# Performance work log

Hardware: AMD Instinct MI355X
Metric: run time of the kernel (lower is better)

## Reference

```python
import jax, jax.numpy as jnp
import numpy as np

N, F, K = 2048, 256, 4
E = 65536

def setup_inputs() -> dict:
    key = jax.random.key(0)
    ks = jax.random.split(key, 8)
    batch_x = jax.random.normal(ks[0], (N, F), dtype=jnp.float32)
    # eigen-matrix of a normalized Laplacian is diagonal in practice, but the
    # original code treats it as a dense [N,N] operand; we mimic a diagonal
    # eigenvalue matrix (eigenvalues in [0,2]) -- math is identical either way.
    lam_diag = 2.0 * jax.random.uniform(ks[1], (N,), dtype=jnp.float32)
    batch_lam = jnp.diag(lam_diag)
    batch_U = jax.random.normal(ks[2], (N, N), dtype=jnp.float32) / jnp.sqrt(jnp.float32(N))
    # init.uniform_(a, 0, 2) / (b, 0, 2) / (c, -1, 1); keep a-b bounded away from 0
    a_list = 1.0 + jax.random.uniform(ks[3], (K,), dtype=jnp.float32)        # [1,2)
    b_list = 0.9 * jax.random.uniform(ks[4], (K,), dtype=jnp.float32)       # [0,0.9)
    c_list = 2.0 * jax.random.uniform(ks[5], (K,), dtype=jnp.float32) - 1.0  # [-1,1)
    residual_alpha = jnp.ones((1,), dtype=jnp.float32)
    edge_index = jax.random.randint(ks[6], (2, E), 0, N, dtype=jnp.int64)
    return {"batch_x": batch_x, "batch_lam": batch_lam, "batch_U": batch_U,
            "a_list": a_list, "b_list": b_list, "c_list": c_list,
            "residual_alpha": residual_alpha, "edge_index": edge_index}

def reference(batch_x, batch_lam, batch_U, a_list, b_list, c_list, residual_alpha, edge_index):
    n = batch_lam.shape[0]
    I = jnp.eye(n, dtype=batch_lam.dtype)
    out = residual_alpha * batch_x  # residual added at hop 0 in original
    for i in range(a_list.shape[0]):
        # filter_rep = (a_i*I - Lam) @ (Lam - b_i*I), then relu
        rep = (a_list[i] * I - batch_lam) @ (batch_lam - b_list[i] * I)
        rep = jax.nn.relu(rep)
        scale = c_list[i] / ((a_list[i] - b_list[i]) * (a_list[i] - b_list[i]) / 4.0)
        filt = scale * (batch_U @ (rep @ (batch_U.T @ batch_x)))
        out = out + filt
    return out
```

## Files before the change

kernel.cpp:

```cpp
#include <hip/hip_runtime.h>
#include <type_traits>

typedef unsigned short u16;
typedef __attribute__((ext_vector_type(8))) short short8;
typedef __attribute__((ext_vector_type(4))) float floatx4;

__device__ __forceinline__ u16 f2u(float f) {
  unsigned int x = __float_as_uint(f);
  x += 0x7fff + ((x >> 16) & 1);
  return (u16)(x >> 16);
}

__device__ __forceinline__ void async16(const void* g, void* l) {
  __builtin_amdgcn_global_load_lds(
      (const __attribute__((address_space(1))) unsigned int*)g,
      (__attribute__((address_space(3))) unsigned int*)l, 16, 0, 0);
}

__global__ __launch_bounds__(256) void prep_kernel(
    const float* __restrict__ U, const float* __restrict__ x,
    u16* __restrict__ Ut, u16* __restrict__ Ubf, u16* __restrict__ xT,
    int N, int F) {
  __shared__ __attribute__((aligned(16))) float tile[64][65];
  int bb = blockIdx.x;
  int t = threadIdx.x;

  const float* in;
  u16 *outT, *outC;
  int R, C, c0, r0;
  if (bb < 1024) {
    in = U; outT = Ut; outC = Ubf; R = N; C = N;
    c0 = (bb & 31) * 64; r0 = (bb >> 5) * 64;
  } else {
    int b2 = bb - 1024;
    in = x; outT = xT; outC = nullptr; R = N; C = F;
    c0 = (b2 & 3) * 64; r0 = (b2 >> 2) * 64;
  }

#pragma unroll
  for (int p = 0; p < 4; ++p) {
    int e = p * 256 + t;
    int row = e >> 4, col = (e & 15) * 4;
    float4 v = *(const float4*)(in + (size_t)(r0 + row) * C + c0 + col);
    tile[row][col] = v.x;
    tile[row][col + 1] = v.y;
    tile[row][col + 2] = v.z;
    tile[row][col + 3] = v.w;
    if (outC) {
      union { uint2 u; u16 s[4]; } pk;
      pk.s[0] = f2u(v.x); pk.s[1] = f2u(v.y);
      pk.s[2] = f2u(v.z); pk.s[3] = f2u(v.w);
      *(uint2*)(outC + (size_t)(r0 + row) * C + c0 + col) = pk.u;
    }
  }
  __syncthreads();
#pragma unroll
  for (int p = 0; p < 2; ++p) {
    int e = p * 256 + t;
    int orow = e >> 3, oc = (e & 7) * 8;
    union { uint4 v; u16 s[8]; } tmp;
#pragma unroll
    for (int i = 0; i < 8; ++i) tmp.s[i] = f2u(tile[oc + i][orow]);
    *(uint4*)(outT + (size_t)(c0 + orow) * R + r0 + oc) = tmp.v;
  }
}

template <bool WIDE_N, bool SCALE_D, bool RESIDUAL, typename CT>
__global__ __launch_bounds__(256) void gemm32(
    const u16* __restrict__ A, const u16* __restrict__ B, CT* __restrict__ C,
    int M, int NN, int K, const float* __restrict__ lam,
    const float* __restrict__ pa, const float* __restrict__ pb,
    const float* __restrict__ pc, const float* __restrict__ resid,
    const float* __restrict__ alpha_p) {
  __shared__ __attribute__((aligned(16))) u16 lA[2 * 8192];
  __shared__ __attribute__((aligned(16))) u16 lB[2 * 8192];
  const int b = blockIdx.x;
  int m0, n0;
  if (WIDE_N) {
    m0 = ((b >> 3) & 7) * 32;
    n0 = ((b & 7) * 8 + (b >> 6)) * 32;
  } else {
    m0 = ((b & 7) * 8 + (b >> 6)) * 32;
    n0 = ((b >> 3) & 7) * 32;
  }
  const int t = threadIdx.x;
  const int wave = t >> 6, lane = t & 63;
  const int wm = wave >> 1, wn = wave & 1;
  const int q = lane >> 4, l15 = lane & 15;

  const int within = t & 127, st0 = t >> 7;
  const u16* gA = A + (size_t)(m0 + (within >> 2)) * K + (within & 3) * 8;
  const u16* gB = B + (size_t)(n0 + (within >> 2)) * K + (within & 3) * 8;
  char* lAc = (char*)lA;
  char* lBc = (char*)lB;

  const int NM = K >> 8;

  auto issue = [&](int i, int buf) {
    int k0 = i * 256;
#pragma unroll
    for (int p = 0; p < 4; ++p) {
      int st = 2 * p + st0;
      async16(gA + k0 + st * 32, lAc + buf * 16384 + p * 4096 + t * 16);
      async16(gB + k0 + st * 32, lBc + buf * 16384 + p * 4096 + t * 16);
    }
  };

  floatx4 acc = (floatx4){0.f, 0.f, 0.f, 0.f};

  issue(0, 0);
  for (int i = 0; i < NM; ++i) {
    const int buf = i & 1;
    __syncthreads();
    if (i + 1 < NM) issue(i + 1, buf ^ 1);
    const u16* lAb = lA + buf * 8192;
    const u16* lBb = lB + buf * 8192;
#pragma unroll
    for (int st = 0; st < 8; ++st) {
      short8 af = *(const short8*)&lAb[st * 1024 + (wm * 16 + l15) * 32 + q * 8];
      short8 bf = *(const short8*)&lBb[st * 1024 + (wn * 16 + l15) * 32 + q * 8];
      acc = __builtin_amdgcn_mfma_f32_16x16x32_bf16(af, bf, acc, 0, 0, 0);
    }
  }

  const int col = n0 + wn * 16 + l15;
  float ds = 1.f;
  if (SCALE_D) {
    float lv = lam[(size_t)col * NN + col];
    float dacc = 0.f;
#pragma unroll
    for (int i = 0; i < 4; ++i) {
      float ai = pa[i], bi = pb[i], ci = pc[i];
      float rep = (ai - lv) * (lv - bi);
      rep = rep > 0.f ? rep : 0.f;
      dacc += ci * 4.f / ((ai - bi) * (ai - bi)) * rep;
    }
    ds = dacc;
  }
  float alpha = 0.f;
  if (RESIDUAL) alpha = alpha_p[0];
  const int rbase = m0 + wm * 16 + q * 4;
#pragma unroll
  for (int r = 0; r < 4; ++r) {
    float v = acc[r];
    if (SCALE_D) v *= ds;
    size_t idx = (size_t)(rbase + r) * NN + col;
    if (RESIDUAL) v += alpha * resid[idx];
    if constexpr (std::is_same<CT, u16>::value)
      C[idx] = f2u(v);
    else
      C[idx] = v;
  }
}

extern "C" void kernel_launch(void* const* d_in, const int* in_sizes, int n_in,
                              void* d_out, int out_size, void* d_ws,
                              size_t ws_size, hipStream_t stream) {
  const int N = 2048, F = 256;
  const float* x = (const float*)d_in[0];
  const float* lam = (const float*)d_in[1];
  const float* U = (const float*)d_in[2];
  const float* a = (const float*)d_in[3];
  const float* b = (const float*)d_in[4];
  const float* c = (const float*)d_in[5];
  const float* alpha = (const float*)d_in[6];

  char* ws = (char*)d_ws;
  u16* xT = (u16*)ws;
  u16* Ut = (u16*)(ws + (1 << 20));
  u16* Ubf = (u16*)(ws + (9 << 20));
  u16* zT = (u16*)(ws + (17 << 20));

  prep_kernel<<<1152, 256, 0, stream>>>(U, x, Ut, Ubf, xT, N, F);
  gemm32<true, true, false, u16><<<512, 256, 0, stream>>>(
      xT, Ut, zT, F, N, N, lam, a, b, c, nullptr, nullptr);
  gemm32<false, false, true, float><<<512, 256, 0, stream>>>(
      Ubf, zT, (float*)d_out, N, F, N, nullptr, nullptr, nullptr, nullptr,
      x, alpha);
}
```

Baseline: 108.9 us.

## Split K across waves with LDS reduction and XOR-swizzle shared memory layout

```diff
diff --git a/kernel.cpp b/kernel.cpp
--- a/kernel.cpp
+++ b/kernel.cpp
@@ -85,12 +85,13 @@
   }
   const int t = threadIdx.x;
   const int wave = t >> 6, lane = t & 63;
-  const int wm = wave >> 1, wn = wave & 1;
   const int q = lane >> 4, l15 = lane & 15;
 
   const int within = t & 127, st0 = t >> 7;
-  const u16* gA = A + (size_t)(m0 + (within >> 2)) * K + (within & 3) * 8;
-  const u16* gB = B + (size_t)(n0 + (within >> 2)) * K + (within & 3) * 8;
+  const int srow = within >> 2;
+  const int schunk = (within & 3) ^ ((srow >> 1) & 3);
+  const u16* gA = A + (size_t)(m0 + srow) * K + schunk * 8;
+  const u16* gB = B + (size_t)(n0 + srow) * K + schunk * 8;
   char* lAc = (char*)lA;
   char* lBc = (char*)lB;
 
@@ -106,7 +107,13 @@
     }
   };
 
-  floatx4 acc = (floatx4){0.f, 0.f, 0.f, 0.f};
+  floatx4 acc[2][2];
+#pragma unroll
+  for (int m = 0; m < 2; ++m)
+#pragma unroll
+    for (int n = 0; n < 2; ++n) acc[m][n] = (floatx4){0.f, 0.f, 0.f, 0.f};
+
+  const int ksw = (q ^ ((l15 >> 1) & 3)) * 8;
 
   issue(0, 0);
   for (int i = 0; i < NM; ++i) {
@@ -116,17 +123,42 @@
     const u16* lAb = lA + buf * 8192;
     const u16* lBb = lB + buf * 8192;
 #pragma unroll
-    for (int st = 0; st < 8; ++st) {
-      short8 af = *(const short8*)&lAb[st * 1024 + (wm * 16 + l15) * 32 + q * 8];
-      short8 bf = *(const short8*)&lBb[st * 1024 + (wn * 16 + l15) * 32 + q * 8];
-      acc = __builtin_amdgcn_mfma_f32_16x16x32_bf16(af, bf, acc, 0, 0, 0);
-    }
-  }
-
-  const int col = n0 + wn * 16 + l15;
+    for (int ss = 0; ss < 2; ++ss) {
+      const int st = 2 * wave + ss;
+      const u16* As = lAb + st * 1024;
+      const u16* Bs = lBb + st * 1024;
+      short8 af[2], bf[2];
+#pragma unroll
+      for (int m = 0; m < 2; ++m)
+        af[m] = *(const short8*)&As[(m * 16 + l15) * 32 + ksw];
+#pragma unroll
+      for (int n = 0; n < 2; ++n)
+        bf[n] = *(const short8*)&Bs[(n * 16 + l15) * 32 + ksw];
+#pragma unroll
+      for (int m = 0; m < 2; ++m)
+#pragma unroll
+        for (int n = 0; n < 2; ++n)
+          acc[m][n] =
+              __builtin_amdgcn_mfma_f32_16x16x32_bf16(af[m], bf[n], acc[m][n], 0, 0, 0);
+    }
+  }
+
+  __syncthreads();
+  float* red = (float*)lA;
+#pragma unroll
+  for (int m = 0; m < 2; ++m)
+#pragma unroll
+    for (int n = 0; n < 2; ++n)
+#pragma unroll
+      for (int r = 0; r < 4; ++r)
+        red[wave * 1024 + (m * 16 + q * 4 + r) * 32 + n * 16 + l15] = acc[m][n][r];
+  __syncthreads();
+
+  const int col = t & 31;
   float ds = 1.f;
   if (SCALE_D) {
-    float lv = lam[(size_t)col * NN + col];
+    const int ac = n0 + col;
+    float lv = lam[(size_t)ac * NN + ac];
     float dacc = 0.f;
 #pragma unroll
     for (int i = 0; i < 4; ++i) {
@@ -139,12 +171,13 @@
   }
   float alpha = 0.f;
   if (RESIDUAL) alpha = alpha_p[0];
-  const int rbase = m0 + wm * 16 + q * 4;
-#pragma unroll
-  for (int r = 0; r < 4; ++r) {
-    float v = acc[r];
+#pragma unroll
+  for (int p = 0; p < 4; ++p) {
+    const int row = (t >> 5) + p * 8;
+    const int e = row * 32 + col;
+    float v = red[e] + red[1024 + e] + red[2048 + e] + red[3072 + e];
     if (SCALE_D) v *= ds;
-    size_t idx = (size_t)(rbase + r) * NN + col;
+    size_t idx = (size_t)(m0 + row) * NN + (n0 + col);
     if (RESIDUAL) v += alpha * resid[idx];
     if constexpr (std::is_same<CT, u16>::value)
       C[idx] = f2u(v);
```

New measurement: 107.1 us, median of 2. Within noise of the previous version (-1.6%).
